# Kernel optimization log

Measured on AMD Instinct MI355X. Metric: run time of the kernel, lower is better.

The kernel has to match this reference:

```python
import jax, jax.numpy as jnp
import numpy as np

TOP_K = 8
CAPACITY = 512  # >> mean load (T*K/E = 256); overflow probability is negligible

def _silu(x):
    return x * jax.nn.sigmoid(x)

def setup_inputs() -> dict:
    key = jax.random.key(0)
    ks = jax.random.split(key, 7)
    B, S, H, E, I, Is = 2, 1024, 1024, 64, 512, 2048
    s = 0.05
    return {
        "hidden_states": jax.random.normal(ks[0], (B, S, H), jnp.float32),
        "gate_w": jax.random.normal(ks[1], (H, E), jnp.float32) * s,
        "shared_gate_w": jax.random.normal(ks[2], (H, 1), jnp.float32) * s,
        "shared_gate_up_w": jax.random.normal(ks[3], (H, 2 * Is), jnp.float32) * s,
        "shared_down_w": jax.random.normal(ks[4], (Is, H), jnp.float32) * s,
        "expert_gate_up_w": jax.random.normal(ks[5], (E, H, 2 * I), jnp.float32) * s,
        "expert_down_w": jax.random.normal(ks[6], (E, I, H), jnp.float32) * s,
    }

def reference(hidden_states, gate_w, shared_gate_w, shared_gate_up_w, shared_down_w, expert_gate_up_w, expert_down_w):
    B, S, H = hidden_states.shape
    x = hidden_states.reshape(-1, H)                      # [T,H]
    T = x.shape[0]
    E = gate_w.shape[1]
    Is = shared_gate_up_w.shape[1] // 2
    I = expert_gate_up_w.shape[2] // 2

    # ---- shared expert (SwiGLU) with sigmoid token gate ----
    gu = x @ shared_gate_up_w                              # [T,2Is]
    shared = (_silu(gu[:, :Is]) * gu[:, Is:]) @ shared_down_w
    shared = shared * jax.nn.sigmoid(x @ shared_gate_w)    # [T,H]

    # ---- router: fp32 softmax -> top-k -> renormalize ----
    logits = x @ gate_w                                    # [T,E]
    probs = jax.nn.softmax(logits.astype(jnp.float32), axis=-1)
    w, idx = jax.lax.top_k(probs, TOP_K)                   # [T,K]
    w = (w / jnp.sum(w, axis=-1, keepdims=True)).astype(x.dtype)

    # ---- dispatch tokens to per-expert buffers (gather/scatter) ----
    e_flat = idx.reshape(-1)                               # [A] assignments
    w_flat = w.reshape(-1)
    A = e_flat.shape[0]
    tok = jnp.arange(A) // TOP_K                           # source token per assignment
    onehot = jax.nn.one_hot(e_flat, E, dtype=jnp.int32)    # [A,E]
    pos = jnp.take_along_axis(jnp.cumsum(onehot, axis=0) - 1, e_flat[:, None], axis=1)[:, 0]
    slot = jnp.minimum(pos, CAPACITY)                      # overflow -> dummy slot
    buf = jnp.zeros((E, CAPACITY + 1, H), x.dtype).at[e_flat, slot].set(x[tok])

    # ---- grouped expert SwiGLU ----
    gu_e = jnp.einsum('ech,ehf->ecf', buf, expert_gate_up_w)   # [E,C+1,2I]
    act = _silu(gu_e[..., :I]) * gu_e[..., I:]
    out_e = jnp.einsum('eci,eih->ech', act, expert_down_w)     # [E,C+1,H]

    # ---- combine ----
    y = out_e[e_flat, slot] * w_flat[:, None]              # [A,H]
    y = jnp.where((pos < CAPACITY)[:, None], y, jnp.zeros_like(y))
    y = y.reshape(T, TOP_K, H).sum(axis=1)                 # [T,H]

    return (y + shared).reshape(B, S, H)
```

## Files before the change

### kernel.cpp

```cpp
#include <hip/hip_runtime.h>
#include <math.h>

#define T_TOK 2048
#define H_DIM 1024
#define E_NUM 64
#define KTOP 8
#define CAP  512
#define I_DIM 512
#define IS_DIM 2048
#define BK 64

typedef __attribute__((ext_vector_type(8))) _Float16 half8;
typedef __attribute__((ext_vector_type(4))) _Float16 half4v;
typedef __attribute__((ext_vector_type(4))) float f32x4;

__device__ __forceinline__ float sigm(float x){ return 1.f/(1.f+__expf(-x)); }

__device__ __forceinline__ void gl16(const _Float16* g, _Float16* l) {
  __builtin_amdgcn_global_load_lds((const __attribute__((address_space(1))) void*)g,
                                   (__attribute__((address_space(3))) void*)l,
                                   16, 0, 0);
}

__global__ __launch_bounds__(256)
void k_tcvt(const float* __restrict__ S, _Float16* __restrict__ D, int K, int N)
{
  __shared__ float T[64][65];
  const size_t so = (size_t)blockIdx.z*K*N;
  const int n0 = blockIdx.x*64, k0 = blockIdx.y*64;
  const int tid = threadIdx.x;
  #pragma unroll
  for (int i=0;i<4;++i){
    int id = tid + i*256;
    int r = id >> 4, c = (id & 15)*4;
    float4 v = *(const float4*)(S + so + (size_t)(k0+r)*N + n0 + c);
    T[r][c]=v.x; T[r][c+1]=v.y; T[r][c+2]=v.z; T[r][c+3]=v.w;
  }
  __syncthreads();
  #pragma unroll
  for (int i=0;i<2;++i){
    int id = tid + i*256;
    int n = id >> 3, kc = (id & 7)*8;
    half8 h;
    #pragma unroll
    for (int j=0;j<8;++j) h[j] = (_Float16)T[kc+j][n];
    *(half8*)(D + so + (size_t)(n0+n)*K + k0 + kc) = h;
  }
}

__global__ __launch_bounds__(256)
void k_cvtx(const float* __restrict__ X, _Float16* __restrict__ Xh)
{
  size_t i = ((size_t)blockIdx.x*256 + threadIdx.x)*4;
  float4 v = *(const float4*)(X + i);
  half4v h = { (_Float16)v.x, (_Float16)v.y, (_Float16)v.z, (_Float16)v.w };
  *(half4v*)(Xh + i) = h;
}

__global__ __launch_bounds__(256)
void k_router(const float* __restrict__ X, const float* __restrict__ GW,
              const float* __restrict__ SGW, int* __restrict__ counts,
              int* __restrict__ etok, float* __restrict__ gate_tok,
              int* __restrict__ asg, float* __restrict__ aw)
{
  __shared__ float Xs[4][1024];
  __shared__ float part[4][4][64];
  const int tid = threadIdx.x, w = tid>>6, lane = tid&63;
  const int t0 = blockIdx.x*4;
  #pragma unroll
  for (int i=0;i<4;++i){
    int idx = tid + i*256;
    *(float4*)(&Xs[0][0] + idx*4) = *(const float4*)(X + (size_t)t0*H_DIM + idx*4);
  }
  __syncthreads();
  {
    float a0=0.f,a1=0.f,a2=0.f,a3=0.f;
    const int kb = w*256;
    #pragma unroll 4
    for (int k=0;k<256;++k){
      float gv = GW[(size_t)(kb+k)*E_NUM + lane];
      a0 = fmaf(Xs[0][kb+k], gv, a0);
      a1 = fmaf(Xs[1][kb+k], gv, a1);
      a2 = fmaf(Xs[2][kb+k], gv, a2);
      a3 = fmaf(Xs[3][kb+k], gv, a3);
    }
    part[w][0][lane]=a0; part[w][1][lane]=a1; part[w][2][lane]=a2; part[w][3][lane]=a3;
  }
  float g = 0.f;
  #pragma unroll
  for (int i=0;i<16;++i) g = fmaf(Xs[w][lane+64*i], SGW[lane+64*i], g);
  #pragma unroll
  for (int off=32;off;off>>=1) g += __shfl_xor(g, off);
  __syncthreads();
  const int t = t0 + w;
  if (lane==0) gate_tok[t] = sigm(g);
  float curv = part[0][w][lane]+part[1][w][lane]+part[2][w][lane]+part[3][w][lane];
  float topv[KTOP]; int topi[KTOP];
  #pragma unroll
  for (int r = 0; r < KTOP; ++r) {
    float bv = curv; int bi = lane;
    #pragma unroll
    for (int off = 32; off > 0; off >>= 1) {
      float ov = __shfl_xor(bv, off);
      int oi = __shfl_xor(bi, off);
      if (ov > bv || (ov == bv && oi < bi)) { bv = ov; bi = oi; }
    }
    topv[r] = bv; topi[r] = bi;
    if (lane == bi) curv = -INFINITY;
  }
  if (lane == 0) {
    float m = topv[0], s = 0.f, wv[KTOP];
    #pragma unroll
    for (int r = 0; r < KTOP; ++r){ wv[r] = __expf(topv[r]-m); s += wv[r]; }
    float inv = 1.f/s;
    for (int r = 0; r < KTOP; ++r) {
      int ee = topi[r];
      int pos = atomicAdd(&counts[ee], 1);
      bool ok = (pos < CAP);
      if (ok) etok[ee*CAP + pos] = t;
      asg[t*KTOP + r] = ok ? (ee*CAP + pos) : -1;
      aw[t*KTOP + r]  = wv[r]*inv;
    }
  }
}


template<int MT>
__device__ __forceinline__ void stageA_lin(const _Float16* __restrict__ Ab, int ldk, int k0,
                                           int tid, _Float16* Asb)
{
  const int w = tid>>6, l = tid&63, sub = l>>3, gc = (l&7) ^ sub;
  #pragma unroll
  for (int j=0;j<MT;++j){
    int r = (w*MT + j)*8 + sub;
    gl16(Ab + (size_t)r*ldk + k0 + gc*8, Asb + (w*MT+j)*512 + l*8);
  }
}
__device__ __forceinline__ void stageA_ptr(const _Float16* const* bj, int k0,
                                           int tid, _Float16* Asb)
{
  const int w = tid>>6, l = tid&63, gc = (l&7) ^ (l>>3);
  #pragma unroll
  for (int j=0;j<4;++j)
    gl16(bj[j] + k0 + gc*8, Asb + (w*4+j)*512 + l*8);
}
__device__ __forceinline__ void stageB(const _Float16* __restrict__ Bt, int ldk,
                                       int r0, int r1, int k0, int tid, _Float16* Bsb)
{
  const int w = tid>>6, l = tid&63, sub = l>>3, gc = (l&7) ^ sub;
  #pragma unroll
  for (int j=0;j<4;++j){
    int r = (w*4+j)*8 + sub;
    int grow = (r < 64) ? (r0 + r) : (r1 + r - 64);
    gl16(Bt + (size_t)grow*ldk + k0 + gc*8, Bsb + (w*4+j)*512 + l*8);
  }
}

template<int MT>
__device__ __forceinline__ void mfma_bk64(const _Float16* As, const _Float16* Bs,
                                          int wy, const int* bidx, int lane,
                                          f32x4 acc[][4])
{
  const int lm = lane & 15, q = lane >> 4, h = lm & 7;
  half8 a[2][MT], b[2][4];
  #pragma unroll
  for (int kk=0;kk<2;++kk){
    #pragma unroll
    for (int mt=0;mt<MT;++mt){
      int r = wy*(MT*16) + mt*16 + lm;
      int ch = ((kk<<2)|q) ^ h;
      a[kk][mt] = *(const half8*)(As + r*BK + ch*8);
    }
    #pragma unroll
    for (int nt=0;nt<4;++nt){
      int n = bidx[nt]*16 + lm;
      int ch = ((kk<<2)|q) ^ h;
      b[kk][nt] = *(const half8*)(Bs + n*BK + ch*8);
    }
  }
  #pragma unroll
  for (int kk=0;kk<2;++kk)
    #pragma unroll
    for (int nt=0;nt<4;++nt)
      #pragma unroll
      for (int mt=0;mt<MT;++mt)
        acc[mt][nt] = __builtin_amdgcn_mfma_f32_16x16x32_f16(a[kk][mt], b[kk][nt], acc[mt][nt], 0,0,0);
}

#define ZACC(MT_) \
  f32x4 acc[MT_][4]; \
  _Pragma("unroll") for (int a_=0;a_<MT_;++a_) \
  _Pragma("unroll") for (int b_=0;b_<4;++b_) acc[a_][b_] = (f32x4){0.f,0.f,0.f,0.f};

__global__ __launch_bounds__(256,2)
void k_gu_shared(const _Float16* __restrict__ Xh, const _Float16* __restrict__ Wt,
                 _Float16* __restrict__ O)
{
  __shared__ __align__(16) _Float16 As[2][128*BK];
  __shared__ __align__(16) _Float16 Bs[2][128*BK];
  const int tid = threadIdx.x, lane = tid & 63, wave = tid >> 6;
  const int wx = wave & 1, wy = wave >> 1;
  const int m0 = blockIdx.y * 128, gn0 = blockIdx.x * 64;
  ZACC(4)
  const int bidx[4] = {2*wx, 2*wx+1, 4+2*wx, 5+2*wx};
  const _Float16* Ab = Xh + (size_t)m0*H_DIM;

  stageA_lin<4>(Ab, H_DIM, 0, tid, As[0]);
  stageB(Wt, H_DIM, gn0, IS_DIM+gn0, 0, tid, Bs[0]);
  __syncthreads();
  int cur = 0;
  for (int k0 = 0; k0 < H_DIM; k0 += BK) {
    if (k0 + BK < H_DIM) {
      stageA_lin<4>(Ab, H_DIM, k0+BK, tid, As[cur^1]);
      stageB(Wt, H_DIM, gn0, IS_DIM+gn0, k0+BK, tid, Bs[cur^1]);
    }
    mfma_bk64<4>(As[cur], Bs[cur], wy, bidx, lane, acc);
    __syncthreads();
    cur ^= 1;
  }
  const int lm = lane & 15, q = lane >> 4;
  #pragma unroll
  for (int mt = 0; mt < 4; ++mt) {
    int m = m0 + wy*64 + mt*16 + q*4;
    #pragma unroll
    for (int jj = 0; jj < 2; ++jj) {
      int col = gn0 + (2*wx + jj)*16 + lm;
      #pragma unroll
      for (int r = 0; r < 4; ++r) {
        float g = acc[mt][jj][r], u = acc[mt][2+jj][r];
        O[(size_t)(m + r)*IS_DIM + col] = (_Float16)(g * sigm(g) * u);
      }
    }
  }
}

__global__ __launch_bounds__(256,3)
void k_dn_shared(const _Float16* __restrict__ S, const _Float16* __restrict__ Wt,
                 const float* __restrict__ gate_tok, float* __restrict__ OUT)
{
  __shared__ __align__(16) _Float16 As[2][64*BK];
  __shared__ __align__(16) _Float16 Bs[2][128*BK];
  const int tid = threadIdx.x, lane = tid & 63, wave = tid >> 6;
  const int wx = wave & 1, wy = wave >> 1;
  const int m0 = blockIdx.y * 64, n0 = blockIdx.x * 128;
  ZACC(2)
  const int bidx[4] = {4*wx, 4*wx+1, 4*wx+2, 4*wx+3};
  const _Float16* Ab = S + (size_t)m0*IS_DIM;

  stageA_lin<2>(Ab, IS_DIM, 0, tid, As[0]);
  stageB(Wt, IS_DIM, n0, n0+64, 0, tid, Bs[0]);
  __syncthreads();
  int cur = 0;
  for (int k0 = 0; k0 < IS_DIM; k0 += BK) {
    if (k0 + BK < IS_DIM) {
      stageA_lin<2>(Ab, IS_DIM, k0+BK, tid, As[cur^1]);
      stageB(Wt, IS_DIM, n0, n0+64, k0+BK, tid, Bs[cur^1]);
    }
    mfma_bk64<2>(As[cur], Bs[cur], wy, bidx, lane, acc);
    __syncthreads();
    cur ^= 1;
  }
  const int lm = lane & 15, q = lane >> 4;
  #pragma unroll
  for (int mt = 0; mt < 2; ++mt) {
    int m = m0 + wy*32 + mt*16 + q*4;
    #pragma unroll
    for (int r = 0; r < 4; ++r) {
      float gt = gate_tok[m + r];
      #pragma unroll
      for (int nt = 0; nt < 4; ++nt) {
        int col = n0 + wx*64 + nt*16 + lm;
        OUT[(size_t)(m + r)*H_DIM + col] = acc[mt][nt][r] * gt;
      }
    }
  }
}

__global__ __launch_bounds__(256,2)
void k_gu_expert(const _Float16* __restrict__ Xh, const _Float16* __restrict__ Wt,
                 const int* __restrict__ counts, const int* __restrict__ etok,
                 const _Float16* __restrict__ zp, _Float16* __restrict__ O)
{
  const int e = blockIdx.z;
  int cnt = counts[e]; if (cnt > CAP) cnt = CAP;
  const int m0 = blockIdx.y * 128;
  if (m0 >= cnt) return;
  __shared__ __align__(16) _Float16 As[2][128*BK];
  __shared__ __align__(16) _Float16 Bs[2][128*BK];
  const int tid = threadIdx.x, lane = tid & 63, wave = tid >> 6;
  const int wx = wave & 1, wy = wave >> 1;
  const int gn0 = blockIdx.x * 64;
  ZACC(4)
  const int bidx[4] = {2*wx, 2*wx+1, 4+2*wx, 5+2*wx};
  const _Float16* Wb = Wt + (size_t)e*H_DIM*(2*I_DIM);

  const _Float16* bj[4];
  {
    const int w = tid>>6, l = tid&63, sub = l>>3;
    #pragma unroll
    for (int j=0;j<4;++j){
      int m = m0 + (w*4+j)*8 + sub;
      int t = (m < cnt) ? etok[e*CAP + m] : -1;
      bj[j] = (t >= 0) ? (Xh + (size_t)t*H_DIM) : zp;
    }
  }
  stageA_ptr(bj, 0, tid, As[0]);
  stageB(Wb, H_DIM, gn0, I_DIM+gn0, 0, tid, Bs[0]);
  __syncthreads();
  int cur = 0;
  for (int k0 = 0; k0 < H_DIM; k0 += BK) {
    if (k0 + BK < H_DIM) {
      stageA_ptr(bj, k0+BK, tid, As[cur^1]);
      stageB(Wb, H_DIM, gn0, I_DIM+gn0, k0+BK, tid, Bs[cur^1]);
    }
    mfma_bk64<4>(As[cur], Bs[cur], wy, bidx, lane, acc);
    __syncthreads();
    cur ^= 1;
  }
  const int lm = lane & 15, q = lane >> 4;
  #pragma unroll
  for (int mt = 0; mt < 4; ++mt) {
    int m = m0 + wy*64 + mt*16 + q*4;
    #pragma unroll
    for (int jj = 0; jj < 2; ++jj) {
      int col = gn0 + (2*wx + jj)*16 + lm;
      #pragma unroll
      for (int r = 0; r < 4; ++r) {
        if (m + r < cnt) {
          float g = acc[mt][jj][r], u = acc[mt][2+jj][r];
          O[((size_t)e*CAP + m + r)*I_DIM + col] = (_Float16)(g * sigm(g) * u);
        }
      }
    }
  }
}

__global__ __launch_bounds__(256,2)
void k_dn_expert(const _Float16* __restrict__ G, const _Float16* __restrict__ Wt,
                 const int* __restrict__ counts, const _Float16* __restrict__ zp,
                 float* __restrict__ Oe)
{
  const int e = blockIdx.z;
  int cnt = counts[e]; if (cnt > CAP) cnt = CAP;
  const int m0 = blockIdx.y * 128;
  if (m0 >= cnt) return;
  const int n0 = blockIdx.x * 128;
  __shared__ __align__(16) _Float16 As[2][128*BK];
  __shared__ __align__(16) _Float16 Bs[2][128*BK];
  const int tid = threadIdx.x, lane = tid & 63, wave = tid >> 6;
  const int wx = wave & 1, wy = wave >> 1;
  ZACC(4)
  const int bidx[4] = {4*wx, 4*wx+1, 4*wx+2, 4*wx+3};
  const _Float16* Wb = Wt + (size_t)e*I_DIM*H_DIM;

  const _Float16* bj[4];
  {
    const int w = tid>>6, l = tid&63, sub = l>>3;
    #pragma unroll
    for (int j=0;j<4;++j){
      int m = m0 + (w*4+j)*8 + sub;
      bj[j] = (m < cnt) ? (G + (size_t)(e*CAP + m)*I_DIM) : zp;
    }
  }
  stageA_ptr(bj, 0, tid, As[0]);
  stageB(Wb, I_DIM, n0, n0+64, 0, tid, Bs[0]);
  __syncthreads();
  int cur = 0;
  for (int k0 = 0; k0 < I_DIM; k0 += BK) {
    if (k0 + BK < I_DIM) {
      stageA_ptr(bj, k0+BK, tid, As[cur^1]);
      stageB(Wb, I_DIM, n0, n0+64, k0+BK, tid, Bs[cur^1]);
    }
    mfma_bk64<4>(As[cur], Bs[cur], wy, bidx, lane, acc);
    __syncthreads();
    cur ^= 1;
  }
  const int lm = lane & 15, q = lane >> 4;
  #pragma unroll
  for (int mt = 0; mt < 4; ++mt) {
    int m = m0 + wy*64 + mt*16 + q*4;
    #pragma unroll
    for (int r = 0; r < 4; ++r) {
      if (m + r < cnt) {
        #pragma unroll
        for (int nt = 0; nt < 4; ++nt) {
          int col = n0 + wx*64 + nt*16 + lm;
          Oe[(size_t)(e*CAP + m + r)*H_DIM + col] = acc[mt][nt][r];
        }
      }
    }
  }
}

__global__ __launch_bounds__(256)
void k_combine(const float* __restrict__ Oe, const int* __restrict__ asg,
               const float* __restrict__ aw, float* __restrict__ OUT)
{
  __shared__ int sa[KTOP]; __shared__ float sw[KTOP];
  const int t = blockIdx.x, tid = threadIdx.x;
  if (tid < KTOP){ sa[tid] = asg[t*KTOP + tid]; sw[tid] = aw[t*KTOP + tid]; }
  __syncthreads();
  float4 acc = *(const float4*)(OUT + (size_t)t*H_DIM + tid*4);
  #pragma unroll
  for (int r = 0; r < KTOP; ++r) {
    int a = sa[r];
    if (a >= 0) {
      float wv = sw[r];
      float4 v = *(const float4*)(Oe + (size_t)a*H_DIM + tid*4);
      acc.x = fmaf(v.x, wv, acc.x); acc.y = fmaf(v.y, wv, acc.y);
      acc.z = fmaf(v.z, wv, acc.z); acc.w = fmaf(v.w, wv, acc.w);
    }
  }
  *(float4*)(OUT + (size_t)t*H_DIM + tid*4) = acc;
}

extern "C" void kernel_launch(void* const* d_in, const int* in_sizes, int n_in,
                              void* d_out, int out_size, void* d_ws, size_t ws_size,
                              hipStream_t stream) {
  const float* x    = (const float*)d_in[0];
  const float* gw   = (const float*)d_in[1];
  const float* sgw  = (const float*)d_in[2];
  const float* sguw = (const float*)d_in[3];
  const float* sdw  = (const float*)d_in[4];
  const float* eguw = (const float*)d_in[5];
  const float* edw  = (const float*)d_in[6];
  float* out = (float*)d_out;

  char* ws = (char*)d_ws;
  int*      counts   = (int*)(ws + 0);
  _Float16* zp       = (_Float16*)(ws + 4096);
  int*      etok     = (int*)(ws + 32768);
  int*      asg      = (int*)(ws + 163840);
  float*    aw       = (float*)(ws + 229376);
  float*    gate_tok = (float*)(ws + 294912);
  _Float16* Xh       = (_Float16*)(ws + (1u<<20));
  _Float16* plane    = (_Float16*)(ws + (8u<<20));
  _Float16* actg     = (_Float16*)(ws + (16u<<20));
  float*    Oe       = (float*)(ws + (48u<<20));
  _Float16* sguwT    = (_Float16*)(ws + (176u<<20));
  _Float16* sdwT     = (_Float16*)(ws + (184u<<20));
  _Float16* eguwT    = (_Float16*)(ws + (192u<<20));
  _Float16* edwT     = (_Float16*)(ws + (320u<<20));

  hipMemsetAsync(ws, 0, 32768, stream);
  k_cvtx<<<T_TOK*H_DIM/1024, 256, 0, stream>>>(x, Xh);
  k_router<<<T_TOK/4, 256, 0, stream>>>(x, gw, sgw, counts, etok, gate_tok, asg, aw);
  k_tcvt<<<dim3(4096/64, 1024/64, 1),  256, 0, stream>>>(sguw, sguwT, 1024, 4096);
  k_tcvt<<<dim3(1024/64, 2048/64, 1),  256, 0, stream>>>(sdw,  sdwT,  2048, 1024);
  k_tcvt<<<dim3(1024/64, 1024/64, 64), 256, 0, stream>>>(eguw, eguwT, 1024, 1024);
  k_tcvt<<<dim3(1024/64,  512/64, 64), 256, 0, stream>>>(edw,  edwT,   512, 1024);
  k_gu_shared<<<dim3(IS_DIM/64, T_TOK/128), 256, 0, stream>>>(Xh, sguwT, plane);
  k_dn_shared<<<dim3(H_DIM/128, T_TOK/64), 256, 0, stream>>>(plane, sdwT, gate_tok, out);
  k_gu_expert<<<dim3(I_DIM/64, CAP/128, E_NUM), 256, 0, stream>>>(Xh, eguwT, counts, etok, zp, actg);
  k_dn_expert<<<dim3(H_DIM/128, CAP/128, E_NUM), 256, 0, stream>>>(actg, edwT, counts, zp, Oe);
  k_combine<<<T_TOK, 256, 0, stream>>>(Oe, asg, aw, out);
}
```

Baseline: 850.3 us.

## Merge weight transposes, fuse x conversion into router, XCD-remap GEMMs, fp16 expert outputs

All four weight transpose-and-convert launches are merged into one kernel that picks its matrix from a flat block index. The separate fp32-to-fp16 pass over the activations is folded into the router, which already loads those rows. The shared-down and both expert GEMMs remap block indices so that neighbouring tiles of one expert or row band land on the same XCD, which should improve L2 reuse. The expert down-projection output is stored in fp16 instead of fp32, halving its write and combine read traffic at a small precision cost.

```diff
diff --git a/kernel.cpp b/kernel.cpp
--- a/kernel.cpp
+++ b/kernel.cpp
@@ -23,17 +23,39 @@
 }
 
 __global__ __launch_bounds__(256)
-void k_tcvt(const float* __restrict__ S, _Float16* __restrict__ D, int K, int N)
-{
+void k_tcvt_all(const float* __restrict__ eguw, const float* __restrict__ edw,
+                const float* __restrict__ sguw, const float* __restrict__ sdw,
+                _Float16* __restrict__ eguwT, _Float16* __restrict__ edwT,
+                _Float16* __restrict__ sguwT, _Float16* __restrict__ sdwT)
+{
+  const int b = blockIdx.x;
+  const float* S; _Float16* D; int K, N, n0, k0;
+  if (b < 16384) {
+    int e = b >> 8, t = b & 255;
+    K = 1024; N = 1024;
+    S = eguw + (size_t)e*K*N; D = eguwT + (size_t)e*K*N;
+    n0 = (t & 15)*64; k0 = (t >> 4)*64;
+  } else if (b < 24576) {
+    int b2 = b - 16384; int e = b2 >> 7, t = b2 & 127;
+    K = 512; N = 1024;
+    S = edw + (size_t)e*K*N; D = edwT + (size_t)e*K*N;
+    n0 = (t & 15)*64; k0 = (t >> 4)*64;
+  } else if (b < 25600) {
+    int b2 = b - 24576;
+    K = 1024; N = 4096; S = sguw; D = sguwT;
+    n0 = (b2 & 63)*64; k0 = (b2 >> 6)*64;
+  } else {
+    int b2 = b - 25600;
+    K = 2048; N = 1024; S = sdw; D = sdwT;
+    n0 = (b2 & 15)*64; k0 = (b2 >> 4)*64;
+  }
   __shared__ float T[64][65];
-  const size_t so = (size_t)blockIdx.z*K*N;
-  const int n0 = blockIdx.x*64, k0 = blockIdx.y*64;
   const int tid = threadIdx.x;
   #pragma unroll
   for (int i=0;i<4;++i){
     int id = tid + i*256;
     int r = id >> 4, c = (id & 15)*4;
-    float4 v = *(const float4*)(S + so + (size_t)(k0+r)*N + n0 + c);
+    float4 v = *(const float4*)(S + (size_t)(k0+r)*N + n0 + c);
     T[r][c]=v.x; T[r][c+1]=v.y; T[r][c+2]=v.z; T[r][c+3]=v.w;
   }
   __syncthreads();
@@ -44,24 +66,16 @@
     half8 h;
     #pragma unroll
     for (int j=0;j<8;++j) h[j] = (_Float16)T[kc+j][n];
-    *(half8*)(D + so + (size_t)(n0+n)*K + k0 + kc) = h;
-  }
-}
-
-__global__ __launch_bounds__(256)
-void k_cvtx(const float* __restrict__ X, _Float16* __restrict__ Xh)
-{
-  size_t i = ((size_t)blockIdx.x*256 + threadIdx.x)*4;
-  float4 v = *(const float4*)(X + i);
-  half4v h = { (_Float16)v.x, (_Float16)v.y, (_Float16)v.z, (_Float16)v.w };
-  *(half4v*)(Xh + i) = h;
+    *(half8*)(D + (size_t)(n0+n)*K + k0 + kc) = h;
+  }
 }
 
 __global__ __launch_bounds__(256)
 void k_router(const float* __restrict__ X, const float* __restrict__ GW,
               const float* __restrict__ SGW, int* __restrict__ counts,
               int* __restrict__ etok, float* __restrict__ gate_tok,
-              int* __restrict__ asg, float* __restrict__ aw)
+              int* __restrict__ asg, float* __restrict__ aw,
+              _Float16* __restrict__ Xh)
 {
   __shared__ float Xs[4][1024];
   __shared__ float part[4][4][64];
@@ -70,7 +84,10 @@
   #pragma unroll
   for (int i=0;i<4;++i){
     int idx = tid + i*256;
-    *(float4*)(&Xs[0][0] + idx*4) = *(const float4*)(X + (size_t)t0*H_DIM + idx*4);
+    float4 v = *(const float4*)(X + (size_t)t0*H_DIM + idx*4);
+    *(float4*)(&Xs[0][0] + idx*4) = v;
+    half4v h = {(_Float16)v.x,(_Float16)v.y,(_Float16)v.z,(_Float16)v.w};
+    *(half4v*)(Xh + (size_t)t0*H_DIM + idx*4) = h;
   }
   __syncthreads();
   {
@@ -242,7 +259,9 @@
   __shared__ __align__(16) _Float16 Bs[2][128*BK];
   const int tid = threadIdx.x, lane = tid & 63, wave = tid >> 6;
   const int wx = wave & 1, wy = wave >> 1;
-  const int m0 = blockIdx.y * 64, n0 = blockIdx.x * 128;
+  const int lin = blockIdx.x + (blockIdx.y<<3);
+  const int xcd = lin & 7, q0 = lin >> 3;
+  const int m0 = ((xcd<<2) + (q0>>3)) * 64, n0 = (q0 & 7) * 128;
   ZACC(2)
   const int bidx[4] = {4*wx, 4*wx+1, 4*wx+2, 4*wx+3};
   const _Float16* Ab = S + (size_t)m0*IS_DIM;
@@ -281,15 +300,17 @@
                  const int* __restrict__ counts, const int* __restrict__ etok,
                  const _Float16* __restrict__ zp, _Float16* __restrict__ O)
 {
-  const int e = blockIdx.z;
+  const int lin = blockIdx.x + ((blockIdx.y + (blockIdx.z<<2))<<3);
+  const int xcd = lin & 7, q0 = lin >> 3;
+  const int e = xcd + ((q0 >> 5) << 3);
+  const int m0 = ((q0 >> 3) & 3) * 128;
+  const int gn0 = (q0 & 7) * 64;
   int cnt = counts[e]; if (cnt > CAP) cnt = CAP;
-  const int m0 = blockIdx.y * 128;
   if (m0 >= cnt) return;
   __shared__ __align__(16) _Float16 As[2][128*BK];
   __shared__ __align__(16) _Float16 Bs[2][128*BK];
   const int tid = threadIdx.x, lane = tid & 63, wave = tid >> 6;
   const int wx = wave & 1, wy = wave >> 1;
-  const int gn0 = blockIdx.x * 64;
   ZACC(4)
   const int bidx[4] = {2*wx, 2*wx+1, 4+2*wx, 5+2*wx};
   const _Float16* Wb = Wt + (size_t)e*H_DIM*(2*I_DIM);
@@ -338,13 +359,15 @@
 __global__ __launch_bounds__(256,2)
 void k_dn_expert(const _Float16* __restrict__ G, const _Float16* __restrict__ Wt,
                  const int* __restrict__ counts, const _Float16* __restrict__ zp,
-                 float* __restrict__ Oe)
-{
-  const int e = blockIdx.z;
+                 _Float16* __restrict__ Oe)
+{
+  const int lin = blockIdx.x + ((blockIdx.y + (blockIdx.z<<2))<<3);
+  const int xcd = lin & 7, q0 = lin >> 3;
+  const int e = xcd + ((q0 >> 5) << 3);
+  const int m0 = ((q0 >> 3) & 3) * 128;
+  const int n0 = (q0 & 7) * 128;
   int cnt = counts[e]; if (cnt > CAP) cnt = CAP;
-  const int m0 = blockIdx.y * 128;
   if (m0 >= cnt) return;
-  const int n0 = blockIdx.x * 128;
   __shared__ __align__(16) _Float16 As[2][128*BK];
   __shared__ __align__(16) _Float16 Bs[2][128*BK];
   const int tid = threadIdx.x, lane = tid & 63, wave = tid >> 6;
@@ -385,7 +408,7 @@
         #pragma unroll
         for (int nt = 0; nt < 4; ++nt) {
           int col = n0 + wx*64 + nt*16 + lm;
-          Oe[(size_t)(e*CAP + m + r)*H_DIM + col] = acc[mt][nt][r];
+          Oe[(size_t)(e*CAP + m + r)*H_DIM + col] = (_Float16)acc[mt][nt][r];
         }
       }
     }
@@ -393,7 +416,7 @@
 }
 
 __global__ __launch_bounds__(256)
-void k_combine(const float* __restrict__ Oe, const int* __restrict__ asg,
+void k_combine(const _Float16* __restrict__ Oe, const int* __restrict__ asg,
                const float* __restrict__ aw, float* __restrict__ OUT)
 {
   __shared__ int sa[KTOP]; __shared__ float sw[KTOP];
@@ -406,9 +429,9 @@
     int a = sa[r];
     if (a >= 0) {
       float wv = sw[r];
-      float4 v = *(const float4*)(Oe + (size_t)a*H_DIM + tid*4);
-      acc.x = fmaf(v.x, wv, acc.x); acc.y = fmaf(v.y, wv, acc.y);
-      acc.z = fmaf(v.z, wv, acc.z); acc.w = fmaf(v.w, wv, acc.w);
+      half4v v = *(const half4v*)(Oe + (size_t)a*H_DIM + tid*4);
+      acc.x = fmaf((float)v[0], wv, acc.x); acc.y = fmaf((float)v[1], wv, acc.y);
+      acc.z = fmaf((float)v[2], wv, acc.z); acc.w = fmaf((float)v[3], wv, acc.w);
     }
   }
   *(float4*)(OUT + (size_t)t*H_DIM + tid*4) = acc;
@@ -436,19 +459,15 @@
   _Float16* Xh       = (_Float16*)(ws + (1u<<20));
   _Float16* plane    = (_Float16*)(ws + (8u<<20));
   _Float16* actg     = (_Float16*)(ws + (16u<<20));
-  float*    Oe       = (float*)(ws + (48u<<20));
+  _Float16* Oe       = (_Float16*)(ws + (48u<<20));
   _Float16* sguwT    = (_Float16*)(ws + (176u<<20));
   _Float16* sdwT     = (_Float16*)(ws + (184u<<20));
   _Float16* eguwT    = (_Float16*)(ws + (192u<<20));
   _Float16* edwT     = (_Float16*)(ws + (320u<<20));
 
   hipMemsetAsync(ws, 0, 32768, stream);
-  k_cvtx<<<T_TOK*H_DIM/1024, 256, 0, stream>>>(x, Xh);
-  k_router<<<T_TOK/4, 256, 0, stream>>>(x, gw, sgw, counts, etok, gate_tok, asg, aw);
-  k_tcvt<<<dim3(4096/64, 1024/64, 1),  256, 0, stream>>>(sguw, sguwT, 1024, 4096);
-  k_tcvt<<<dim3(1024/64, 2048/64, 1),  256, 0, stream>>>(sdw,  sdwT,  2048, 1024);
-  k_tcvt<<<dim3(1024/64, 1024/64, 64), 256, 0, stream>>>(eguw, eguwT, 1024, 1024);
-  k_tcvt<<<dim3(1024/64,  512/64, 64), 256, 0, stream>>>(edw,  edwT,   512, 1024);
+  k_router<<<T_TOK/4, 256, 0, stream>>>(x, gw, sgw, counts, etok, gate_tok, asg, aw, Xh);
+  k_tcvt_all<<<26112, 256, 0, stream>>>(eguw, edw, sguw, sdw, eguwT, edwT, sguwT, sdwT);
   k_gu_shared<<<dim3(IS_DIM/64, T_TOK/128), 256, 0, stream>>>(Xh, sguwT, plane);
   k_dn_shared<<<dim3(H_DIM/128, T_TOK/64), 256, 0, stream>>>(plane, sdwT, gate_tok, out);
   k_gu_expert<<<dim3(I_DIM/64, CAP/128, E_NUM), 256, 0, stream>>>(Xh, eguwT, counts, etok, zp, actg);
```

New measurement: 778.4 us. -8.5%, faster.
